# Performance work log

Hardware: AMD Instinct MI355X
Metric: run time of the kernel (lower is better)

## Reference

```python
import jax, jax.numpy as jnp
import numpy as np

B, I, H = 8192, 1024, 1024

def setup_inputs() -> dict:
    key = jax.random.key(0)
    ks = jax.random.split(key, 6)
    s_in = 1.0 / np.sqrt(I)
    s_h = 1.0 / np.sqrt(H)
    return {
        "x": jax.random.normal(ks[0], (B, I), jnp.float32),
        "h_prev": jax.random.normal(ks[1], (B, H), jnp.float32),
        "c_prev": jax.random.normal(ks[2], (B, H), jnp.float32),
        "Wx": jax.random.normal(ks[3], (4, H, I), jnp.float32) * s_in,   # gate order: input, forget, cell, output
        "Wh": jax.random.normal(ks[4], (4, H, H), jnp.float32) * s_h,
        "bh": jax.random.normal(ks[5], (4, H), jnp.float32) * s_h,
    }

def reference(x, h_prev, c_prev, Wx, Wh, bh):
    # Fused: 2 batched GEMMs for all 4 gates -> [B, 4, H]
    gates = (jnp.einsum('bi,ghi->bgh', x, Wx)
             + jnp.einsum('bk,ghk->bgh', h_prev, Wh)
             + bh[None, :, :])
    i = jax.nn.sigmoid(gates[:, 0])
    f = jax.nn.sigmoid(gates[:, 1])
    g = jnp.tanh(gates[:, 2])
    o = jax.nn.sigmoid(gates[:, 3])
    c_next = f * c_prev + i * g
    h_next = o * jnp.tanh(c_next)
    return (h_next, c_next)
```

## Files before the change

### kernel.cpp

```cpp
#include <hip/hip_runtime.h>
#include <hip/hip_bf16.h>
#include <stdint.h>

#define B_DIM 8192
#define I_DIM 1024
#define H_DIM 1024

typedef __attribute__((ext_vector_type(8))) short short8;
typedef __attribute__((ext_vector_type(4))) float f32x4;

static __device__ __forceinline__ short f2b(float f) {
    __bf16 h = (__bf16)f;
    return __builtin_bit_cast(short, h);
}

static __device__ __forceinline__ short8 pack8(float4 a, float4 b) {
    short8 s;
    s[0] = f2b(a.x); s[1] = f2b(a.y); s[2] = f2b(a.z); s[3] = f2b(a.w);
    s[4] = f2b(b.x); s[5] = f2b(b.y); s[6] = f2b(b.z); s[7] = f2b(b.w);
    return s;
}

static __device__ __forceinline__ float sigmoid_f(float x) {
    return 1.0f / (1.0f + __expf(-x));
}

static __device__ __forceinline__ float tanh_fast(float x) {
    x = fminf(fmaxf(x, -15.0f), 15.0f);
    float e = __expf(2.0f * x);
    return (e - 1.0f) / (e + 1.0f);
}

static __device__ __forceinline__ void load_lds16(const void* gptr, void* lptr) {
    __builtin_amdgcn_global_load_lds(
        (const __attribute__((address_space(1))) uint32_t*)gptr,
        (__attribute__((address_space(3))) uint32_t*)lptr, 16, 0, 0);
}

#define GA_GROUPS (512 * 32 * 2 * 64)
#define GB_GROUPS (256 * 32 * 2 * 64)

__global__ __launch_bounds__(256) void convert_kernel(
    const float* __restrict__ x, const float* __restrict__ h,
    const float* __restrict__ wx, const float* __restrict__ wh,
    short* __restrict__ Aw, short* __restrict__ Bw)
{
    const int64_t total = (int64_t)GA_GROUPS + GB_GROUPS;
    for (int64_t g = (int64_t)blockIdx.x * blockDim.x + threadIdx.x; g < total;
         g += (int64_t)gridDim.x * blockDim.x) {
        const float* src;
        short* dst;
        if (g < GA_GROUPS) {
            const int lane = (int)(g & 63);
            const int rest = (int)(g >> 6);
            const int kh   = rest & 1;
            const int tk   = (rest >> 1) & 31;
            const int mfrag = rest >> 6;
            const int row = (mfrag << 4) + (lane & 15);
            const int k   = (tk << 6) + (kh << 5) + ((lane >> 4) << 3);
            src = (k < 1024) ? (x + (size_t)row * 1024 + k)
                             : (h + (size_t)row * 1024 + (k - 1024));
            dst = Aw + (size_t)g * 8;
        } else {
            const int64_t gb = g - GA_GROUPS;
            const int lane = (int)(gb & 63);
            const int rest = (int)(gb >> 6);
            const int kh   = rest & 1;
            const int tk   = (rest >> 1) & 31;
            const int nfrag = rest >> 6;
            const int cf   = nfrag & 15;
            const int bn   = nfrag >> 4;
            const int gate = cf & 3;
            const int col  = (bn << 6) + ((cf >> 2) << 4) + (lane & 15);
            const int k    = (tk << 6) + (kh << 5) + ((lane >> 4) << 3);
            src = (k < 1024) ? (wx + ((size_t)(gate << 10) + col) * 1024 + k)
                             : (wh + ((size_t)(gate << 10) + col) * 1024 + (k - 1024));
            dst = Bw + (size_t)gb * 8;
        }
        float4 v0 = ((const float4*)src)[0];
        float4 v1 = ((const float4*)src)[1];
        *(short8*)dst = pack8(v0, v1);
    }
}

#define AOFF(d, f) ((d) * 8192 + (f) * 512)
#define BOFF(d, f) ((d) * 8192 + 4096 + (f) * 512)

__global__ __launch_bounds__(256, 4) void lstm_gemm_tlp_kernel(
    const short* __restrict__ Aw, const short* __restrict__ Bw,
    const float* __restrict__ cprev, const float* __restrict__ bh,
    float* __restrict__ out)
{
    __shared__ __align__(16) short smem[16384];

    const int bid = blockIdx.x;
    const int xcd = bid & 7;
    const int c   = bid >> 3;
    const int bm  = c >> 2;
    const int ht  = 4 * xcd + (c & 3);
    const int m0  = bm * 128;

    const int t    = threadIdx.x;
    const int lane = t & 63;
    const int w    = t >> 6;
    const int wm   = w >> 1;
    const int wn   = w & 1;
    const int lc   = lane & 15;

    const short* aSrc0 = Aw + (size_t)(bm * 8 + 2 * w)     * 32768 + lane * 8;
    const short* aSrc1 = Aw + (size_t)(bm * 8 + 2 * w + 1) * 32768 + lane * 8;
    const short* bSrc0 = Bw + (size_t)(ht * 8 + 2 * w)     * 32768 + lane * 8;
    const short* bSrc1 = Bw + (size_t)(ht * 8 + 2 * w + 1) * 32768 + lane * 8;

    f32x4 acc[4][4] = {};

    load_lds16(aSrc0, &smem[AOFF(0, 2 * w)]);
    load_lds16(aSrc1, &smem[AOFF(0, 2 * w + 1)]);
    load_lds16(bSrc0, &smem[BOFF(0, 2 * w)]);
    load_lds16(bSrc1, &smem[BOFF(0, 2 * w + 1)]);
    asm volatile("s_waitcnt vmcnt(0)" ::: "memory");
    __builtin_amdgcn_s_barrier();

#define TILE(d, tp) do { \
    short8 bv[4], av[4]; \
    _Pragma("unroll") \
    for (int j = 0; j < 4; ++j) \
        bv[j] = *(const short8*)&smem[BOFF(d, wn * 4 + j) + lane * 8]; \
    _Pragma("unroll") \
    for (int i = 0; i < 4; ++i) \
        av[i] = *(const short8*)&smem[AOFF(d, wm * 4 + i) + lane * 8]; \
    load_lds16(aSrc0 + (tp) * 512, &smem[AOFF(d ^ 1, 2 * w)]); \
    load_lds16(aSrc1 + (tp) * 512, &smem[AOFF(d ^ 1, 2 * w + 1)]); \
    load_lds16(bSrc0 + (tp) * 512, &smem[BOFF(d ^ 1, 2 * w)]); \
    load_lds16(bSrc1 + (tp) * 512, &smem[BOFF(d ^ 1, 2 * w + 1)]); \
    __builtin_amdgcn_s_setprio(1); \
    _Pragma("unroll") \
    for (int i = 0; i < 4; ++i) \
        _Pragma("unroll") \
        for (int j = 0; j < 4; ++j) \
            acc[i][j] = __builtin_amdgcn_mfma_f32_16x16x32_bf16( \
                av[i], bv[j], acc[i][j], 0, 0, 0); \
    __builtin_amdgcn_s_setprio(0); \
    asm volatile("s_waitcnt vmcnt(0)" ::: "memory"); \
    __builtin_amdgcn_s_barrier(); \
} while (0)

    #pragma unroll 1
    for (int tk2 = 0; tk2 < 32; ++tk2) {
        const int t1 = 2 * tk2 + 1;
        const int t2 = (t1 + 1 < 64) ? t1 + 1 : t1;
        TILE(0, t1);
        TILE(1, t2);
    }
#undef TILE

    const int rg = lane >> 4;
    const int h  = ht * 32 + wn * 16 + lc;
    const float b_i = bh[0 * H_DIM + h];
    const float b_f = bh[1 * H_DIM + h];
    const float b_g = bh[2 * H_DIM + h];
    const float b_o = bh[3 * H_DIM + h];

    #pragma unroll
    for (int mf = 0; mf < 4; ++mf) {
        #pragma unroll
        for (int r = 0; r < 4; ++r) {
            const int row = m0 + wm * 64 + mf * 16 + rg * 4 + r;
            const float pi = acc[mf][0][r] + b_i;
            const float pf = acc[mf][1][r] + b_f;
            const float pg = acc[mf][2][r] + b_g;
            const float po = acc[mf][3][r] + b_o;
            const float iv = sigmoid_f(pi);
            const float fv = sigmoid_f(pf);
            const float gv = tanh_fast(pg);
            const float ov = sigmoid_f(po);
            const float cp = cprev[(size_t)row * H_DIM + h];
            const float cn = fv * cp + iv * gv;
            const float hn = ov * tanh_fast(cn);
            out[(size_t)row * H_DIM + h] = hn;
            out[(size_t)B_DIM * H_DIM + (size_t)row * H_DIM + h] = cn;
        }
    }
}

static __device__ __forceinline__ int swz(int row, int k) {
    int byte = (row << 7) + (k << 1);
    byte ^= (row & 7) << 4;
    return byte >> 1;
}

__global__ __launch_bounds__(256, 2) void lstm_fallback_kernel(
    const float* __restrict__ x, const float* __restrict__ hprev,
    const float* __restrict__ cprev, const float* __restrict__ Wx,
    const float* __restrict__ Wh, const float* __restrict__ bh,
    float* __restrict__ out)
{
    __shared__ __align__(16) short As[128 * 64];
    __shared__ __align__(16) short Bs[128 * 64];

    int bid = blockIdx.x;
    bid = (bid & 7) * 256 + (bid >> 3);
    const int mt = bid >> 5;
    const int ht = bid & 31;
    const int m0 = mt * 128;
    const int h0 = ht * 32;

    const int t    = threadIdx.x;
    const int lane = t & 63;
    const int w    = t >> 6;
    const int wr   = w >> 1;
    const int wc   = w & 1;

    const int srow = t >> 3;
    const int sk   = (t & 7) * 8;

    f32x4 acc[4][4] = {};

    #pragma unroll 1
    for (int phase = 0; phase < 2; ++phase) {
        const float* __restrict__ Ap = phase ? hprev : x;
        const float* __restrict__ Bp = phase ? Wh : Wx;
        #pragma unroll 1
        for (int kk = 0; kk < 1024; kk += 64) {
            __syncthreads();
            #pragma unroll
            for (int p = 0; p < 4; ++p) {
                const int row = srow + p * 32;
                const float4* src = (const float4*)(Ap + (size_t)(m0 + row) * I_DIM + kk + sk);
                *(short8*)&As[swz(row, sk)] = pack8(src[0], src[1]);
            }
            #pragma unroll
            for (int p = 0; p < 4; ++p) {
                const int n    = srow + p * 32;
                const int gate = (n >> 4) & 3;
                const int hcol = h0 + ((n >> 6) << 4) + (n & 15);
                const float4* src = (const float4*)(Bp + (size_t)((gate << 10) + hcol) * 1024 + kk + sk);
                *(short8*)&Bs[swz(n, sk)] = pack8(src[0], src[1]);
            }
            __syncthreads();
            #pragma unroll
            for (int ks = 0; ks < 2; ++ks) {
                const int kb = ks * 32 + ((lane >> 4) << 3);
                short8 a[4], b[4];
                #pragma unroll
                for (int m = 0; m < 4; ++m)
                    a[m] = *(const short8*)&As[swz(wr * 64 + m * 16 + (lane & 15), kb)];
                #pragma unroll
                for (int j = 0; j < 4; ++j)
                    b[j] = *(const short8*)&Bs[swz(wc * 64 + j * 16 + (lane & 15), kb)];
                #pragma unroll
                for (int m = 0; m < 4; ++m)
                    #pragma unroll
                    for (int j = 0; j < 4; ++j)
                        acc[m][j] = __builtin_amdgcn_mfma_f32_16x16x32_bf16(a[m], b[j], acc[m][j], 0, 0, 0);
            }
        }
    }

    const int cl = lane & 15;
    const int rg = lane >> 4;
    const int h  = h0 + wc * 16 + cl;
    const float b_i = bh[0 * H_DIM + h];
    const float b_f = bh[1 * H_DIM + h];
    const float b_g = bh[2 * H_DIM + h];
    const float b_o = bh[3 * H_DIM + h];

    #pragma unroll
    for (int m = 0; m < 4; ++m) {
        #pragma unroll
        for (int r = 0; r < 4; ++r) {
            const int row = m0 + wr * 64 + m * 16 + rg * 4 + r;
            const float pi = acc[m][0][r] + b_i;
            const float pf = acc[m][1][r] + b_f;
            const float pg = acc[m][2][r] + b_g;
            const float po = acc[m][3][r] + b_o;
            const float iv = sigmoid_f(pi);
            const float fv = sigmoid_f(pf);
            const float gv = tanh_fast(pg);
            const float ov = sigmoid_f(po);
            const float cp = cprev[(size_t)row * H_DIM + h];
            const float cn = fv * cp + iv * gv;
            const float hn = ov * tanh_fast(cn);
            out[(size_t)row * H_DIM + h] = hn;
            out[(size_t)B_DIM * H_DIM + (size_t)row * H_DIM + h] = cn;
        }
    }
}

extern "C" void kernel_launch(void* const* d_in, const int* in_sizes, int n_in,
                              void* d_out, int out_size, void* d_ws, size_t ws_size,
                              hipStream_t stream) {
    const float* x     = (const float*)d_in[0];
    const float* hprev = (const float*)d_in[1];
    const float* cprev = (const float*)d_in[2];
    const float* Wx    = (const float*)d_in[3];
    const float* Wh    = (const float*)d_in[4];
    const float* bh    = (const float*)d_in[5];
    float* out = (float*)d_out;

    const size_t need = ((size_t)B_DIM * 2048 + (size_t)4096 * 2048) * sizeof(short);
    if (ws_size >= need && d_ws != nullptr) {
        short* Aw = (short*)d_ws;
        short* Bw = Aw + (size_t)512 * 32768;
        hipLaunchKernelGGL(convert_kernel, dim3(4096), dim3(256), 0, stream,
                           x, hprev, Wx, Wh, Aw, Bw);
        hipLaunchKernelGGL(lstm_gemm_tlp_kernel, dim3(2048), dim3(256), 0, stream,
                           Aw, Bw, cprev, bh, out);
    } else {
        hipLaunchKernelGGL(lstm_fallback_kernel, dim3(2048), dim3(256), 0, stream,
                           x, hprev, cprev, Wx, Wh, bh, out);
    }
}
```

Measured before the change: 152.2 us.

## Load B fragments directly from global into registers, keep only A in LDS

The weight (B) tile no longer goes through LDS. Each wave loads its four B fragments straight from global memory into registers, double-buffered across iterations. LDS use halves and LDS read/write traffic for B is removed. In exchange, B data is fetched redundantly by the two waves that share the same wn (more global/L2 traffic), and register pressure rises from the extra double-buffered fragments.

```diff
diff --git a/kernel.cpp b/kernel.cpp
--- a/kernel.cpp
+++ b/kernel.cpp
@@ -83,15 +83,14 @@
     }
 }
 
-#define AOFF(d, f) ((d) * 8192 + (f) * 512)
-#define BOFF(d, f) ((d) * 8192 + 4096 + (f) * 512)
-
-__global__ __launch_bounds__(256, 4) void lstm_gemm_tlp_kernel(
+#define AOFF(d, f) ((d) * 4096 + (f) * 512)
+
+__global__ __launch_bounds__(256, 4) void lstm_gemm_bd_kernel(
     const short* __restrict__ Aw, const short* __restrict__ Bw,
     const float* __restrict__ cprev, const float* __restrict__ bh,
     float* __restrict__ out)
 {
-    __shared__ __align__(16) short smem[16384];
+    __shared__ __align__(16) short smem[8192];
 
     const int bid = blockIdx.x;
     const int xcd = bid & 7;
@@ -109,37 +108,36 @@
 
     const short* aSrc0 = Aw + (size_t)(bm * 8 + 2 * w)     * 32768 + lane * 8;
     const short* aSrc1 = Aw + (size_t)(bm * 8 + 2 * w + 1) * 32768 + lane * 8;
-    const short* bSrc0 = Bw + (size_t)(ht * 8 + 2 * w)     * 32768 + lane * 8;
-    const short* bSrc1 = Bw + (size_t)(ht * 8 + 2 * w + 1) * 32768 + lane * 8;
+    const short* bBase = Bw + (size_t)(ht * 8 + wn * 4) * 32768 + lane * 8;
 
     f32x4 acc[4][4] = {};
+    short8 bvA[4], bvB[4];
 
     load_lds16(aSrc0, &smem[AOFF(0, 2 * w)]);
     load_lds16(aSrc1, &smem[AOFF(0, 2 * w + 1)]);
-    load_lds16(bSrc0, &smem[BOFF(0, 2 * w)]);
-    load_lds16(bSrc1, &smem[BOFF(0, 2 * w + 1)]);
+    #pragma unroll
+    for (int j = 0; j < 4; ++j)
+        bvA[j] = *(const short8*)(bBase + (size_t)j * 32768);
     asm volatile("s_waitcnt vmcnt(0)" ::: "memory");
     __builtin_amdgcn_s_barrier();
 
-#define TILE(d, tp) do { \
-    short8 bv[4], av[4]; \
-    _Pragma("unroll") \
-    for (int j = 0; j < 4; ++j) \
-        bv[j] = *(const short8*)&smem[BOFF(d, wn * 4 + j) + lane * 8]; \
+#define TILE(d, tp, BC, BN) do { \
+    short8 av[4]; \
     _Pragma("unroll") \
     for (int i = 0; i < 4; ++i) \
         av[i] = *(const short8*)&smem[AOFF(d, wm * 4 + i) + lane * 8]; \
     load_lds16(aSrc0 + (tp) * 512, &smem[AOFF(d ^ 1, 2 * w)]); \
     load_lds16(aSrc1 + (tp) * 512, &smem[AOFF(d ^ 1, 2 * w + 1)]); \
-    load_lds16(bSrc0 + (tp) * 512, &smem[BOFF(d ^ 1, 2 * w)]); \
-    load_lds16(bSrc1 + (tp) * 512, &smem[BOFF(d ^ 1, 2 * w + 1)]); \
+    _Pragma("unroll") \
+    for (int j = 0; j < 4; ++j) \
+        BN[j] = *(const short8*)(bBase + (size_t)j * 32768 + (size_t)(tp) * 512); \
     __builtin_amdgcn_s_setprio(1); \
     _Pragma("unroll") \
     for (int i = 0; i < 4; ++i) \
         _Pragma("unroll") \
         for (int j = 0; j < 4; ++j) \
             acc[i][j] = __builtin_amdgcn_mfma_f32_16x16x32_bf16( \
-                av[i], bv[j], acc[i][j], 0, 0, 0); \
+                av[i], BC[j], acc[i][j], 0, 0, 0); \
     __builtin_amdgcn_s_setprio(0); \
     asm volatile("s_waitcnt vmcnt(0)" ::: "memory"); \
     __builtin_amdgcn_s_barrier(); \
@@ -148,9 +146,9 @@
     #pragma unroll 1
     for (int tk2 = 0; tk2 < 32; ++tk2) {
         const int t1 = 2 * tk2 + 1;
-        const int t2 = (t1 + 1 < 64) ? t1 + 1 : t1;
-        TILE(0, t1);
-        TILE(1, t2);
+        const int t2 = (t1 + 1 < 64) ? t1 + 1 : 63;
+        TILE(0, t1, bvA, bvB);
+        TILE(1, t2, bvB, bvA);
     }
 #undef TILE
 
@@ -304,7 +302,7 @@
         short* Bw = Aw + (size_t)512 * 32768;
         hipLaunchKernelGGL(convert_kernel, dim3(4096), dim3(256), 0, stream,
                            x, hprev, Wx, Wh, Aw, Bw);
-        hipLaunchKernelGGL(lstm_gemm_tlp_kernel, dim3(2048), dim3(256), 0, stream,
+        hipLaunchKernelGGL(lstm_gemm_bd_kernel, dim3(2048), dim3(256), 0, stream,
                            Aw, Bw, cprev, bh, out);
     } else {
         hipLaunchKernelGGL(lstm_fallback_kernel, dim3(2048), dim3(256), 0, stream,
```

Result: slower. 164.1 us (+7.8%).

## Triple-buffer LDS tiles with counted vmcnt waits in LSTM GEMM

Applied to the files above, without the earlier changes.

Moves the GEMM main loop from double-buffered LDS to a three-stage ring buffer, keeping two tile loads in flight and waiting with vmcnt(4) instead of draining all loads before each barrier. The goal is to hide global-to-LDS latency behind MFMA work. In exchange, LDS per block grows from 32 KB to 48 KB and the launch-bounds occupancy hint drops from 4 to 3 blocks, which reduces latency hiding through parallel blocks. The tail issues redundant reloads of tile 63.

```diff
diff --git a/kernel.cpp b/kernel.cpp
--- a/kernel.cpp
+++ b/kernel.cpp
@@ -86,12 +86,12 @@
 #define AOFF(d, f) ((d) * 8192 + (f) * 512)
 #define BOFF(d, f) ((d) * 8192 + 4096 + (f) * 512)
 
-__global__ __launch_bounds__(256, 4) void lstm_gemm_tlp_kernel(
+__global__ __launch_bounds__(256, 3) void lstm_gemm_cnt_kernel(
     const short* __restrict__ Aw, const short* __restrict__ Bw,
     const float* __restrict__ cprev, const float* __restrict__ bh,
     float* __restrict__ out)
 {
-    __shared__ __align__(16) short smem[16384];
+    __shared__ __align__(16) short smem[24576];
 
     const int bid = blockIdx.x;
     const int xcd = bid & 7;
@@ -114,25 +114,23 @@
 
     f32x4 acc[4][4] = {};
 
-    load_lds16(aSrc0, &smem[AOFF(0, 2 * w)]);
-    load_lds16(aSrc1, &smem[AOFF(0, 2 * w + 1)]);
-    load_lds16(bSrc0, &smem[BOFF(0, 2 * w)]);
-    load_lds16(bSrc1, &smem[BOFF(0, 2 * w + 1)]);
-    asm volatile("s_waitcnt vmcnt(0)" ::: "memory");
-    __builtin_amdgcn_s_barrier();
-
-#define TILE(d, tp) do { \
+#define STAGE(db, tp) \
+    load_lds16(aSrc0 + (tp) * 512, &smem[AOFF(db, 2 * w)]); \
+    load_lds16(aSrc1 + (tp) * 512, &smem[AOFF(db, 2 * w + 1)]); \
+    load_lds16(bSrc0 + (tp) * 512, &smem[BOFF(db, 2 * w)]); \
+    load_lds16(bSrc1 + (tp) * 512, &smem[BOFF(db, 2 * w + 1)]);
+
+#define TILE(db, sdb, tp) do { \
+    asm volatile("s_waitcnt vmcnt(4)" ::: "memory"); \
+    __builtin_amdgcn_s_barrier(); \
+    STAGE(sdb, tp) \
     short8 bv[4], av[4]; \
     _Pragma("unroll") \
     for (int j = 0; j < 4; ++j) \
-        bv[j] = *(const short8*)&smem[BOFF(d, wn * 4 + j) + lane * 8]; \
+        bv[j] = *(const short8*)&smem[BOFF(db, wn * 4 + j) + lane * 8]; \
     _Pragma("unroll") \
     for (int i = 0; i < 4; ++i) \
-        av[i] = *(const short8*)&smem[AOFF(d, wm * 4 + i) + lane * 8]; \
-    load_lds16(aSrc0 + (tp) * 512, &smem[AOFF(d ^ 1, 2 * w)]); \
-    load_lds16(aSrc1 + (tp) * 512, &smem[AOFF(d ^ 1, 2 * w + 1)]); \
-    load_lds16(bSrc0 + (tp) * 512, &smem[BOFF(d ^ 1, 2 * w)]); \
-    load_lds16(bSrc1 + (tp) * 512, &smem[BOFF(d ^ 1, 2 * w + 1)]); \
+        av[i] = *(const short8*)&smem[AOFF(db, wm * 4 + i) + lane * 8]; \
     __builtin_amdgcn_s_setprio(1); \
     _Pragma("unroll") \
     for (int i = 0; i < 4; ++i) \
@@ -141,18 +139,25 @@
             acc[i][j] = __builtin_amdgcn_mfma_f32_16x16x32_bf16( \
                 av[i], bv[j], acc[i][j], 0, 0, 0); \
     __builtin_amdgcn_s_setprio(0); \
-    asm volatile("s_waitcnt vmcnt(0)" ::: "memory"); \
-    __builtin_amdgcn_s_barrier(); \
 } while (0)
 
+    STAGE(0, 0)
+    STAGE(1, 1)
+
     #pragma unroll 1
-    for (int tk2 = 0; tk2 < 32; ++tk2) {
-        const int t1 = 2 * tk2 + 1;
-        const int t2 = (t1 + 1 < 64) ? t1 + 1 : t1;
-        TILE(0, t1);
-        TILE(1, t2);
-    }
+    for (int tk3 = 0; tk3 < 21; ++tk3) {
+        const int t0 = 3 * tk3;
+        const int p2 = (t0 + 2 < 64) ? t0 + 2 : 63;
+        const int p3 = (t0 + 3 < 64) ? t0 + 3 : 63;
+        const int p4 = (t0 + 4 < 64) ? t0 + 4 : 63;
+        TILE(0, 2, p2);
+        TILE(1, 0, p3);
+        TILE(2, 1, p4);
+    }
+    TILE(0, 2, 63);
 #undef TILE
+#undef STAGE
+    asm volatile("s_waitcnt vmcnt(0)" ::: "memory");
 
     const int rg = lane >> 4;
     const int h  = ht * 32 + wn * 16 + lc;
@@ -304,7 +309,7 @@
         short* Bw = Aw + (size_t)512 * 32768;
         hipLaunchKernelGGL(convert_kernel, dim3(4096), dim3(256), 0, stream,
                            x, hprev, Wx, Wh, Aw, Bw);
-        hipLaunchKernelGGL(lstm_gemm_tlp_kernel, dim3(2048), dim3(256), 0, stream,
+        hipLaunchKernelGGL(lstm_gemm_cnt_kernel, dim3(2048), dim3(256), 0, stream,
                            Aw, Bw, cprev, bh, out);
     } else {
         hipLaunchKernelGGL(lstm_fallback_kernel, dim3(2048), dim3(256), 0, stream,
```

Result: no change. 151.5 us, median of 2 (-0.5%).
